# Kernel tuning notes

Hardware: AMD Instinct MI355X
Metric: run time of the kernel (lower is better)

Reference implementation:

```python
import jax, jax.numpy as jnp
import numpy as np

D_MODEL = 1024
NUM_HEADS = 16
HEAD_DIM = D_MODEL // NUM_HEADS
B, S = 4, 2048


def setup_inputs() -> dict:
    key = jax.random.key(0)
    ks = jax.random.split(key, 11)
    scale = 1.0 / np.sqrt(D_MODEL)
    return {
        "query": jax.random.normal(ks[0], (B, S, D_MODEL), jnp.float32),
        "key": jax.random.normal(ks[1], (B, S, D_MODEL), jnp.float32),
        "value": jax.random.normal(ks[2], (B, S, D_MODEL), jnp.float32),
        "Wq": jax.random.normal(ks[3], (D_MODEL, D_MODEL), jnp.float32) * scale,
        "bq": jnp.zeros((D_MODEL,), jnp.float32),
        "Wk": jax.random.normal(ks[4], (D_MODEL, D_MODEL), jnp.float32) * scale,
        "bk": jnp.zeros((D_MODEL,), jnp.float32),
        "Wv": jax.random.normal(ks[5], (D_MODEL, D_MODEL), jnp.float32) * scale,
        "bv": jnp.zeros((D_MODEL,), jnp.float32),
        "Wo": jax.random.normal(ks[6], (D_MODEL, D_MODEL), jnp.float32) * scale,
        "bo": jnp.zeros((D_MODEL,), jnp.float32),
    }


def reference(query, key, value, Wq, bq, Wk, bk, Wv, bv, Wo, bo):
    b = query.shape[0]
    # nn.Linear: x @ W.T + b; weights stored [out, in]
    def split_heads(x):
        return x.reshape(b, -1, NUM_HEADS, HEAD_DIM).transpose(0, 2, 1, 3)  # [b,h,s,d]
    q = split_heads(query @ Wq.T + bq)
    k = split_heads(key @ Wk.T + bk)
    v = split_heads(value @ Wv.T + bv)
    scores = jnp.einsum("bhqd,bhkd->bhqk", q, k) / np.sqrt(HEAD_DIM)
    weights = jax.nn.softmax(scores, axis=-1)
    out = jnp.einsum("bhqk,bhkd->bhqd", weights, v)
    out = out.transpose(0, 2, 1, 3).reshape(b, -1, D_MODEL)
    return out @ Wo.T + bo
```

## Files before the change

kernel.cpp:

```cpp
#include <hip/hip_runtime.h>

typedef __bf16 bf16;
typedef __bf16 bf16x4 __attribute__((ext_vector_type(4)));
typedef __bf16 bf16x8 __attribute__((ext_vector_type(8)));
typedef float f32x4 __attribute__((ext_vector_type(4)));

#define MFMA16(a, b, c) __builtin_amdgcn_mfma_f32_16x16x32_bf16((a), (b), (c), 0, 0, 0)

#define QSCALE 0.1803368808f

__device__ __forceinline__ void async_cp16(const bf16* g, bf16* l) {
    __builtin_amdgcn_global_load_lds((const __attribute__((address_space(1))) void*)g,
                                     (__attribute__((address_space(3))) void*)l, 16, 0, 0);
}

struct CvtArgs { const float* src[7]; bf16* dst[7]; };
__global__ void cvt_all(CvtArgs a) {
    int bx = blockIdx.x, t, off;
    if (bx < 12288) { t = bx >> 12;            off = bx & 4095; }
    else            { t = 3 + ((bx - 12288) >> 9); off = (bx - 12288) & 511; }
    size_t i = (size_t)off * 256 + threadIdx.x;
    const float4* p = (const float4*)(a.src[t] + i * 8);
    float4 x = p[0], y = p[1];
    bf16x8 o;
    o[0] = (bf16)x.x; o[1] = (bf16)x.y; o[2] = (bf16)x.z; o[3] = (bf16)x.w;
    o[4] = (bf16)y.x; o[5] = (bf16)y.y; o[6] = (bf16)y.z; o[7] = (bf16)y.w;
    *(bf16x8*)(a.dst[t] + i * 8) = o;
}

__device__ __forceinline__ void gemm_core(
    const bf16* __restrict__ A, const bf16* __restrict__ W,
    const float* __restrict__ bias, void* __restrict__ Cout,
    int mode, int m0, int n0)
{
    __shared__ bf16 As[128 * 32];
    __shared__ bf16 Bs[128 * 32];
    const int K = 1024;
    const int tid = threadIdx.x;
    const int lane = tid & 63, wave = tid >> 6;
    const int l15 = lane & 15, quad = lane >> 4;
    const int wm = wave >> 1, wn = wave & 1;

    f32x4 acc[4][4] = {};

    const int r0 = tid >> 2, k8 = (tid & 3) * 8;
    const bf16* Ag0 = A + (size_t)(m0 + r0) * K + k8;
    const bf16* Ag1 = A + (size_t)(m0 + r0 + 64) * K + k8;
    const bf16* Wg0 = W + (size_t)(n0 + r0) * K + k8;
    const bf16* Wg1 = W + (size_t)(n0 + r0 + 64) * K + k8;
    bf16* Al0 = As + tid * 8;
    bf16* Al1 = As + (tid + 256) * 8;
    bf16* Bl0 = Bs + tid * 8;
    bf16* Bl1 = Bs + (tid + 256) * 8;

    for (int k0 = 0; k0 < K; k0 += 32) {
        __syncthreads();
        async_cp16(Ag0 + k0, Al0);
        async_cp16(Ag1 + k0, Al1);
        async_cp16(Wg0 + k0, Bl0);
        async_cp16(Wg1 + k0, Bl1);
        __syncthreads();

        bf16x8 af[4], bfr[4];
#pragma unroll
        for (int t = 0; t < 4; ++t) {
            af[t]  = *(const bf16x8*)(As + (wm * 64 + t * 16 + l15) * 32 + quad * 8);
            bfr[t] = *(const bf16x8*)(Bs + (wn * 64 + t * 16 + l15) * 32 + quad * 8);
        }
#pragma unroll
        for (int mt = 0; mt < 4; ++mt)
#pragma unroll
            for (int nt = 0; nt < 4; ++nt)
                acc[mt][nt] = MFMA16(af[mt], bfr[nt], acc[mt][nt]);
    }

#pragma unroll
    for (int mt = 0; mt < 4; ++mt) {
#pragma unroll
        for (int nt = 0; nt < 4; ++nt) {
            int col = n0 + wn * 64 + nt * 16 + l15;
            float bcol = (mode == 2) ? 0.0f : bias[col];
#pragma unroll
            for (int r = 0; r < 4; ++r) {
                int row = m0 + wm * 64 + mt * 16 + quad * 4 + r;
                float val = acc[mt][nt][r];
                if (mode == 2) {
                    val += bias[row];
                    int bb = col >> 11, s = col & 2047;
                    int u = s & 31;
                    int sp = (s & ~31) | (((u >> 2) & 3) * 8 + (u >> 4) * 4 + (u & 3));
                    ((bf16*)Cout)[((size_t)(bb * 1024 + row) << 11) + sp] = (bf16)val;
                } else if (mode == 3) {
                    ((float*)Cout)[(size_t)row * 1024 + col] = val + bcol;
                } else {
                    val += bcol;
                    if (mode == 0) val *= QSCALE;
                    int bb = row >> 11, s = row & 2047, hh = col >> 6, d = col & 63;
                    ((bf16*)Cout)[(((size_t)(bb * 16 + hh) * 2048 + s) << 6) + d] = (bf16)val;
                }
            }
        }
    }
}

struct QkvArgs {
    const bf16* A[3];
    const bf16* W[3];
    const float* bias[3];
    bf16* out[3];
};

__global__ __launch_bounds__(256) void qkv_gemm(QkvArgs t) {
    int z = blockIdx.y;
    int bx = blockIdx.x;
    int m0, n0;
    if (z < 2) { m0 = (bx & 63) * 128; n0 = (bx >> 6) * 128; }
    else       { m0 = (bx & 7) * 128;  n0 = (bx >> 3) * 128; }
    gemm_core(t.A[z], t.W[z], t.bias[z], t.out[z], z, m0, n0);
}

__global__ __launch_bounds__(256) void oproj_gemm(
    const bf16* __restrict__ A, const bf16* __restrict__ W,
    const float* __restrict__ bias, float* __restrict__ Cout) {
    gemm_core(A, W, bias, Cout, 3, blockIdx.x * 128, blockIdx.y * 128);
}

__global__ __launch_bounds__(256, 2) void attn_kernel(
    const bf16* __restrict__ Qh, const bf16* __restrict__ Kh,
    const bf16* __restrict__ Vtg, bf16* __restrict__ AO)
{
    __shared__ bf16 Kl[64 * 64];
    __shared__ bf16 Vl[64 * 64];

    const int tid = threadIdx.x;
    const int lane = tid & 63, wave = tid >> 6;
    const int l15 = lane & 15, quad = lane >> 4, l7 = l15 & 7;
    const int h = blockIdx.y, b = blockIdx.z;
    const size_t base = (size_t)(b * 16 + h) << 17;
    const int q0 = blockIdx.x * 256 + wave * 64;

    bf16x8 qf[4][2];
#pragma unroll
    for (int qt = 0; qt < 4; ++qt)
#pragma unroll
        for (int ks = 0; ks < 2; ++ks)
            qf[qt][ks] = *(const bf16x8*)(Qh + base + (q0 + qt * 16 + l15) * 64 + ks * 32 + quad * 8);

    f32x4 o[4][4] = {};
    float ls[4] = {};

    const int sr = tid >> 3;
    const int sc0 = ((tid & 7) ^ (sr & 7)) * 8;
    const int sr2 = sr + 32;

    for (int kt = 0; kt < 2048; kt += 64) {
        __syncthreads();
        async_cp16(Kh + base + (size_t)(kt + sr) * 64 + sc0, Kl + tid * 8);
        async_cp16(Kh + base + (size_t)(kt + sr2) * 64 + sc0, Kl + (tid + 256) * 8);
        async_cp16(Vtg + base + (size_t)sr * 2048 + kt + sc0, Vl + tid * 8);
        async_cp16(Vtg + base + (size_t)sr2 * 2048 + kt + sc0, Vl + (tid + 256) * 8);
        __syncthreads();

        bf16x8 kb[2][4];
#pragma unroll
        for (int ks = 0; ks < 2; ++ks)
#pragma unroll
            for (int ktile = 0; ktile < 4; ++ktile)
                kb[ks][ktile] = *(const bf16x8*)(Kl + (ktile * 16 + l15) * 64 + (((ks * 4 + quad) ^ l7) * 8));

        bf16x8 pf[4][2];
#pragma unroll
        for (int qt = 0; qt < 4; ++qt) {
            f32x4 sc[4] = {};
#pragma unroll
            for (int ks = 0; ks < 2; ++ks)
#pragma unroll
                for (int ktile = 0; ktile < 4; ++ktile)
                    sc[ktile] = MFMA16(kb[ks][ktile], qf[qt][ks], sc[ktile]);
            float sum = 0.0f;
#pragma unroll
            for (int kc = 0; kc < 2; ++kc) {
                bf16x8 pk;
#pragma unroll
                for (int t = 0; t < 2; ++t)
#pragma unroll
                    for (int r = 0; r < 4; ++r) {
                        float p = __builtin_amdgcn_exp2f(sc[kc * 2 + t][r]);
                        sum += p;
                        pk[t * 4 + r] = (bf16)p;
                    }
                pf[qt][kc] = pk;
            }
            ls[qt] += sum;
        }

        bf16x8 va[4][2];
#pragma unroll
        for (int dt = 0; dt < 4; ++dt)
#pragma unroll
            for (int kc = 0; kc < 2; ++kc)
                va[dt][kc] = *(const bf16x8*)(Vl + (dt * 16 + l15) * 64 + (((kc * 4 + quad) ^ l7) * 8));

#pragma unroll
        for (int dt = 0; dt < 4; ++dt)
#pragma unroll
            for (int qt = 0; qt < 4; ++qt)
#pragma unroll
                for (int kc = 0; kc < 2; ++kc)
                    o[dt][qt] = MFMA16(va[dt][kc], pf[qt][kc], o[dt][qt]);
    }

#pragma unroll
    for (int qt = 0; qt < 4; ++qt) {
        float l = ls[qt];
        l += __shfl_xor(l, 16, 64);
        l += __shfl_xor(l, 32, 64);
        float inv = 1.0f / l;
        size_t rb = ((size_t)(b * 2048 + q0 + qt * 16 + l15)) * 1024 + h * 64;
#pragma unroll
        for (int dt = 0; dt < 4; ++dt) {
            bf16x4 ov = {(bf16)(o[dt][qt][0] * inv), (bf16)(o[dt][qt][1] * inv),
                         (bf16)(o[dt][qt][2] * inv), (bf16)(o[dt][qt][3] * inv)};
            *(bf16x4*)(AO + rb + dt * 16 + quad * 4) = ov;
        }
    }
}

extern "C" void kernel_launch(void* const* d_in, const int* in_sizes, int n_in,
                              void* d_out, int out_size, void* d_ws, size_t ws_size,
                              hipStream_t stream) {
    const float* q  = (const float*)d_in[0];
    const float* k  = (const float*)d_in[1];
    const float* v  = (const float*)d_in[2];
    const float* Wq = (const float*)d_in[3];
    const float* bq = (const float*)d_in[4];
    const float* Wk = (const float*)d_in[5];
    const float* bk = (const float*)d_in[6];
    const float* Wv = (const float*)d_in[7];
    const float* bv = (const float*)d_in[8];
    const float* Wo = (const float*)d_in[9];
    const float* bo = (const float*)d_in[10];
    float* out = (float*)d_out;

    const size_t NX = (size_t)8192 * 1024;
    const size_t NW = (size_t)1024 * 1024;
    bf16* ws  = (bf16*)d_ws;
    bf16* Xq  = ws;
    bf16* Xk  = Xq + NX;
    bf16* Xv  = Xk + NX;
    bf16* Wqb = Xv + NX;
    bf16* Wkb = Wqb + NW;
    bf16* Wvb = Wkb + NW;
    bf16* Wob = Wvb + NW;
    bf16* Qh  = Wob + NW;
    bf16* Kh  = Qh + NX;
    bf16* Vt  = Kh + NX;
    bf16* AO  = Xq;

    CvtArgs ca;
    ca.src[0] = q;  ca.dst[0] = Xq;
    ca.src[1] = k;  ca.dst[1] = Xk;
    ca.src[2] = v;  ca.dst[2] = Xv;
    ca.src[3] = Wq; ca.dst[3] = Wqb;
    ca.src[4] = Wk; ca.dst[4] = Wkb;
    ca.src[5] = Wv; ca.dst[5] = Wvb;
    ca.src[6] = Wo; ca.dst[6] = Wob;
    cvt_all<<<14336, 256, 0, stream>>>(ca);

    dim3 bb(256, 1, 1);
    QkvArgs t;
    t.A[0] = Xq;  t.W[0] = Wqb; t.bias[0] = bq; t.out[0] = Qh;
    t.A[1] = Xk;  t.W[1] = Wkb; t.bias[1] = bk; t.out[1] = Kh;
    t.A[2] = Wvb; t.W[2] = Xv;  t.bias[2] = bv; t.out[2] = Vt;
    qkv_gemm<<<dim3(512, 3), bb, 0, stream>>>(t);

    attn_kernel<<<dim3(8, 16, 4), bb, 0, stream>>>(Qh, Kh, Vt, AO);

    oproj_gemm<<<dim3(64, 8), bb, 0, stream>>>(AO, Wob, bo, out);
}
```

Measured before the change: 338.1 us.

## Double-buffer LDS tiles with async prefetch in GEMM and attention loops

Result: slower. 376.3 us (+11.3%).

```diff
diff --git a/kernel.cpp b/kernel.cpp
--- a/kernel.cpp
+++ b/kernel.cpp
@@ -33,8 +33,8 @@
     const float* __restrict__ bias, void* __restrict__ Cout,
     int mode, int m0, int n0)
 {
-    __shared__ bf16 As[128 * 32];
-    __shared__ bf16 Bs[128 * 32];
+    __shared__ bf16 As[2][128 * 32];
+    __shared__ bf16 Bs[2][128 * 32];
     const int K = 1024;
     const int tid = threadIdx.x;
     const int lane = tid & 63, wave = tid >> 6;
@@ -48,30 +48,42 @@
     const bf16* Ag1 = A + (size_t)(m0 + r0 + 64) * K + k8;
     const bf16* Wg0 = W + (size_t)(n0 + r0) * K + k8;
     const bf16* Wg1 = W + (size_t)(n0 + r0 + 64) * K + k8;
-    bf16* Al0 = As + tid * 8;
-    bf16* Al1 = As + (tid + 256) * 8;
-    bf16* Bl0 = Bs + tid * 8;
-    bf16* Bl1 = Bs + (tid + 256) * 8;
-
+    const int so0 = tid * 8, so1 = (tid + 256) * 8;
+
+    async_cp16(Ag0, As[0] + so0);
+    async_cp16(Ag1, As[0] + so1);
+    async_cp16(Wg0, Bs[0] + so0);
+    async_cp16(Wg1, Bs[0] + so1);
+
+    int cur = 0;
     for (int k0 = 0; k0 < K; k0 += 32) {
-        __syncthreads();
-        async_cp16(Ag0 + k0, Al0);
-        async_cp16(Ag1 + k0, Al1);
-        async_cp16(Wg0 + k0, Bl0);
-        async_cp16(Wg1 + k0, Bl1);
-        __syncthreads();
+        if (k0 + 32 < K) {
+            const int nxt = cur ^ 1;
+            async_cp16(Ag0 + k0 + 32, As[nxt] + so0);
+            async_cp16(Ag1 + k0 + 32, As[nxt] + so1);
+            async_cp16(Wg0 + k0 + 32, Bs[nxt] + so0);
+            async_cp16(Wg1 + k0 + 32, Bs[nxt] + so1);
+            asm volatile("s_waitcnt vmcnt(4)" ::: "memory");
+        } else {
+            asm volatile("s_waitcnt vmcnt(0)" ::: "memory");
+        }
+        __builtin_amdgcn_s_barrier();
 
         bf16x8 af[4], bfr[4];
 #pragma unroll
         for (int t = 0; t < 4; ++t) {
-            af[t]  = *(const bf16x8*)(As + (wm * 64 + t * 16 + l15) * 32 + quad * 8);
-            bfr[t] = *(const bf16x8*)(Bs + (wn * 64 + t * 16 + l15) * 32 + quad * 8);
+            af[t]  = *(const bf16x8*)(As[cur] + (wm * 64 + t * 16 + l15) * 32 + quad * 8);
+            bfr[t] = *(const bf16x8*)(Bs[cur] + (wn * 64 + t * 16 + l15) * 32 + quad * 8);
         }
 #pragma unroll
         for (int mt = 0; mt < 4; ++mt)
 #pragma unroll
             for (int nt = 0; nt < 4; ++nt)
                 acc[mt][nt] = MFMA16(af[mt], bfr[nt], acc[mt][nt]);
+
+        __builtin_amdgcn_sched_barrier(0);
+        __builtin_amdgcn_s_barrier();
+        cur ^= 1;
     }
 
 #pragma unroll
@@ -129,8 +141,8 @@
     const bf16* __restrict__ Qh, const bf16* __restrict__ Kh,
     const bf16* __restrict__ Vtg, bf16* __restrict__ AO)
 {
-    __shared__ bf16 Kl[64 * 64];
-    __shared__ bf16 Vl[64 * 64];
+    __shared__ bf16 Kl[2][64 * 64];
+    __shared__ bf16 Vl[2][64 * 64];
 
     const int tid = threadIdx.x;
     const int lane = tid & 63, wave = tid >> 6;
@@ -152,21 +164,33 @@
     const int sr = tid >> 3;
     const int sc0 = ((tid & 7) ^ (sr & 7)) * 8;
     const int sr2 = sr + 32;
-
+    const int so0 = tid * 8, so1 = (tid + 256) * 8;
+
+    async_cp16(Kh + base + (size_t)sr * 64 + sc0, Kl[0] + so0);
+    async_cp16(Kh + base + (size_t)sr2 * 64 + sc0, Kl[0] + so1);
+    async_cp16(Vtg + base + (size_t)sr * 2048 + sc0, Vl[0] + so0);
+    async_cp16(Vtg + base + (size_t)sr2 * 2048 + sc0, Vl[0] + so1);
+
+    int cur = 0;
     for (int kt = 0; kt < 2048; kt += 64) {
-        __syncthreads();
-        async_cp16(Kh + base + (size_t)(kt + sr) * 64 + sc0, Kl + tid * 8);
-        async_cp16(Kh + base + (size_t)(kt + sr2) * 64 + sc0, Kl + (tid + 256) * 8);
-        async_cp16(Vtg + base + (size_t)sr * 2048 + kt + sc0, Vl + tid * 8);
-        async_cp16(Vtg + base + (size_t)sr2 * 2048 + kt + sc0, Vl + (tid + 256) * 8);
-        __syncthreads();
+        if (kt + 64 < 2048) {
+            const int nxt = cur ^ 1;
+            async_cp16(Kh + base + (size_t)(kt + 64 + sr) * 64 + sc0, Kl[nxt] + so0);
+            async_cp16(Kh + base + (size_t)(kt + 64 + sr2) * 64 + sc0, Kl[nxt] + so1);
+            async_cp16(Vtg + base + (size_t)sr * 2048 + kt + 64 + sc0, Vl[nxt] + so0);
+            async_cp16(Vtg + base + (size_t)sr2 * 2048 + kt + 64 + sc0, Vl[nxt] + so1);
+            asm volatile("s_waitcnt vmcnt(4)" ::: "memory");
+        } else {
+            asm volatile("s_waitcnt vmcnt(0)" ::: "memory");
+        }
+        __builtin_amdgcn_s_barrier();
 
         bf16x8 kb[2][4];
 #pragma unroll
         for (int ks = 0; ks < 2; ++ks)
 #pragma unroll
             for (int ktile = 0; ktile < 4; ++ktile)
-                kb[ks][ktile] = *(const bf16x8*)(Kl + (ktile * 16 + l15) * 64 + (((ks * 4 + quad) ^ l7) * 8));
+                kb[ks][ktile] = *(const bf16x8*)(Kl[cur] + (ktile * 16 + l15) * 64 + (((ks * 4 + quad) ^ l7) * 8));
 
         bf16x8 pf[4][2];
 #pragma unroll
@@ -199,7 +223,7 @@
         for (int dt = 0; dt < 4; ++dt)
 #pragma unroll
             for (int kc = 0; kc < 2; ++kc)
-                va[dt][kc] = *(const bf16x8*)(Vl + (dt * 16 + l15) * 64 + (((kc * 4 + quad) ^ l7) * 8));
+                va[dt][kc] = *(const bf16x8*)(Vl[cur] + (dt * 16 + l15) * 64 + (((kc * 4 + quad) ^ l7) * 8));
 
 #pragma unroll
         for (int dt = 0; dt < 4; ++dt)
@@ -208,6 +232,10 @@
 #pragma unroll
                 for (int kc = 0; kc < 2; ++kc)
                     o[dt][qt] = MFMA16(va[dt][kc], pf[qt][kc], o[dt][qt]);
+
+        __builtin_amdgcn_sched_barrier(0);
+        __builtin_amdgcn_s_barrier();
+        cur ^= 1;
     }
 
 #pragma unroll
```
